# Kernel optimization log

Measured on AMD Instinct MI355X. Metric: run time of the kernel, lower is better.

Reference implementation:

```python
import jax, jax.numpy as jnp
import numpy as np

B, T, D, H, C = 2048, 512, 1, 50, 2  # batch, seq_len, input_size, hidden_size, num_classes


def setup_inputs() -> dict:
    key = jax.random.key(0)
    ks = jax.random.split(key, 11)
    k = 1.0 / np.sqrt(H)  # torch default init bound
    u = lambda kk, shape: jax.random.uniform(kk, shape, jnp.float32, -k, k)
    return {
        "x": jax.random.normal(ks[0], (B, T, D), jnp.float32),
        "W_ih0": u(ks[1], (4 * H, D)),
        "W_hh0": u(ks[2], (4 * H, H)),
        "b_ih0": u(ks[3], (4 * H,)),
        "b_hh0": u(ks[4], (4 * H,)),
        "W_ih1": u(ks[5], (4 * H, H)),
        "W_hh1": u(ks[6], (4 * H, H)),
        "b_ih1": u(ks[7], (4 * H,)),
        "b_hh1": u(ks[8], (4 * H,)),
        "W_fc": u(ks[9], (C, H)),
        "b_fc": u(ks[10], (C,)),
    }


def _lstm_layer(x, Wih, Whh, bih, bhh):
    # x: [B, T, Din] -> hidden sequence [B, T, H]. PyTorch gate order: i, f, g, o.
    Bn = x.shape[0]
    Hn = Whh.shape[1]
    # precompute input contribution for all timesteps (one big GEMM)
    xg = jnp.einsum('btd,gd->btg', x, Wih) + bih + bhh  # [B, T, 4H]

    def step(carry, xg_t):
        h, c = carry
        g = xg_t + h @ Whh.T  # [B, 4H]
        i, f, gg, o = jnp.split(g, 4, axis=-1)
        i = jax.nn.sigmoid(i)
        f = jax.nn.sigmoid(f)
        gg = jnp.tanh(gg)
        o = jax.nn.sigmoid(o)
        c = f * c + i * gg
        h = o * jnp.tanh(c)
        return (h, c), h

    h0 = jnp.zeros((Bn, Hn), x.dtype)
    c0 = jnp.zeros((Bn, Hn), x.dtype)
    (_, _), hs = jax.lax.scan(step, (h0, c0), jnp.swapaxes(xg, 0, 1))  # hs: [T, B, H]
    return jnp.swapaxes(hs, 0, 1)


def reference(x, W_ih0, W_hh0, b_ih0, b_hh0, W_ih1, W_hh1, b_ih1, b_hh1, W_fc, b_fc):
    h1 = _lstm_layer(x, W_ih0, W_hh0, b_ih0, b_hh0)
    h2 = _lstm_layer(h1, W_ih1, W_hh1, b_ih1, b_hh1)
    # out[:, -1, :] @ W_fc.T + b_fc  (last-timestep hidden -> classifier)
    return h2[:, -1, :] @ W_fc.T + b_fc
```

## Files before the change

### kernel.cpp

```cpp
#include <hip/hip_runtime.h>

#define T_SEQ 512
#define HID   50
#define NB    8
#define BLK   832

typedef float v4f  __attribute__((ext_vector_type(4)));
typedef _Float16 f16;
typedef f16  f16x8 __attribute__((ext_vector_type(8)));


__device__ __forceinline__ f16x8 ldA0(const float* __restrict__ Whh0,
                                      const float* __restrict__ Wih0,
                                      const float* __restrict__ bih0,
                                      const float* __restrict__ bhh0,
                                      int m, int kb) {
    const int u = m >> 2, g = m & 3;
    f16x8 v;
    #pragma unroll
    for (int j = 0; j < 8; ++j) {
        const int k = kb + j;
        float f = 0.f;
        if (u < HID) {
            const int rho = g * HID + u;
            if (k < HID)      f = Whh0[rho * HID + k];
            else if (k == 62) f = Wih0[rho];
            else if (k == 63) f = bih0[rho] + bhh0[rho];
        }
        v[j] = (f16)f;
    }
    return v;
}

__device__ __forceinline__ f16x8 ldA1a(const float* __restrict__ Wih1,
                                       const float* __restrict__ bih1,
                                       const float* __restrict__ bhh1,
                                       int m, int kb) {
    const int u = m >> 2, g = m & 3;
    f16x8 v;
    #pragma unroll
    for (int j = 0; j < 8; ++j) {
        const int k = kb + j;
        float f = 0.f;
        if (u < HID) {
            const int rho = g * HID + u;
            if (k < HID)      f = Wih1[rho * HID + k];
            else if (k == 63) f = bih1[rho] + bhh1[rho];
        }
        v[j] = (f16)f;
    }
    return v;
}

__device__ __forceinline__ f16x8 ldA1b(const float* __restrict__ Whh1,
                                       int m, int kb) {
    const int u = m >> 2, g = m & 3;
    f16x8 v;
    #pragma unroll
    for (int j = 0; j < 8; ++j) {
        const int k = kb + j;
        float f = 0.f;
        if (u < HID && k < HID) f = Whh1[(g * HID + u) * HID + k];
        v[j] = (f16)f;
    }
    return v;
}

#define MFMA16(A, B, C) __builtin_amdgcn_mfma_f32_16x16x32_f16((A), (B), (C), 0, 0, 0)

__global__ __launch_bounds__(BLK, 1)
void lstm2_mfma(const float* __restrict__ x,
                const float* __restrict__ Wih0,
                const float* __restrict__ Whh0,
                const float* __restrict__ bih0,
                const float* __restrict__ bhh0,
                const float* __restrict__ Wih1,
                const float* __restrict__ Whh1,
                const float* __restrict__ bih1,
                const float* __restrict__ bhh1,
                const float* __restrict__ Wfc,
                const float* __restrict__ bfc,
                float* __restrict__ out)
{
    __shared__ __align__(16) f16 BPH [8 * 64 * 8];
    __shared__ f16   xs16[NB][T_SEQ];
    __shared__ float hfin[HID][NB];

    const int tid  = threadIdx.x;
    const int w    = tid >> 6;
    const int lane = tid & 63;
    const int n16  = lane & 15;
    const int quad = lane >> 4;
    const int bb0  = blockIdx.x * NB;

    const float* xg = x + (long)bb0 * T_SEQ;

    for (int i = tid; i < 8 * 64 * 8; i += BLK) BPH[i] = (f16)0.f;
    for (int i = tid; i < NB * T_SEQ; i += BLK) {
        const int n = i >> 9, tt = i & (T_SEQ - 1);
        xs16[n][tt] = (f16)xg[n * T_SEQ + tt];
    }

    const int m   = w * 16 + n16;
    const int kb0 = quad * 8, kb1 = 32 + quad * 8;
    const f16x8 a0 = ldA0(Whh0, Wih0, bih0, bhh0, m, kb0);
    const f16x8 a1 = ldA0(Whh0, Wih0, bih0, bhh0, m, kb1);
    const f16x8 v0 = ldA1a(Wih1, bih1, bhh1, m, kb0);
    const f16x8 v1 = ldA1a(Wih1, bih1, bhh1, m, kb1);
    const f16x8 v2 = ldA1b(Whh1, m, kb0);
    const f16x8 v3 = ldA1b(Whh1, m, kb1);

    __syncthreads();
    if (tid < NB) {
        BPH[(1 * 64 + 48 + tid) * 8 + 7] = (f16)1.f;
        BPH[(1 * 64 + 56 + tid) * 8 + 7] = (f16)1.f;
        BPH[(3 * 64 + 48 + tid) * 8 + 7] = (f16)1.f;
        BPH[(3 * 64 + 56 + tid) * 8 + 7] = (f16)1.f;
        BPH[(3 * 64 + 48 + tid) * 8 + 6] = xs16[tid][0];
        BPH[(3 * 64 + 56 + tid) * 8 + 6] = xs16[tid][0];
    }
    __syncthreads();

    const int  u_    = w * 4 + quad;
    const bool isl0  = (n16 < 8);
    const bool valid = (u_ < HID);
    const int  wbase = (((u_ & 31) >> 3) * 16 + (n16 & 7)) * 8 + (u_ & 7) + (u_ >> 5) * 512;
    float cs = 0.f;
    const f16x8* BPF = (const f16x8*)BPH;
    const v4f CZ = {0.f, 0.f, 0.f, 0.f};

    #pragma clang loop unroll(disable)
    for (int s = 0; s <= T_SEQ; ++s) {
        const int rb = (s + 1) & 1, wb = s & 1;

        const f16x8 B0 = BPF[(2 * rb + 0) * 64 + lane];
        const f16x8 B1 = BPF[(2 * rb + 1) * 64 + lane];
        const f16x8 B2 = BPF[(4 + 2 * wb + 0) * 64 + lane];
        const f16x8 B3 = BPF[(4 + 2 * wb + 1) * 64 + lane];

        v4f C0 = MFMA16(a0, B0, CZ);
        C0 = MFMA16(a1, B1, C0);
        v4f C1h = MFMA16(v0, B0, CZ);
        C1h = MFMA16(v1, B1, C1h);
        v4f C1r = MFMA16(v2, B2, CZ);
        C1r = MFMA16(v3, B3, C1r);

        v4f CC;
        CC.x = isl0 ? C0.x : (C1h.x + C1r.x);
        CC.y = isl0 ? C0.y : (C1h.y + C1r.y);
        CC.z = isl0 ? C0.z : (C1h.z + C1r.z);
        CC.w = isl0 ? C0.w : (C1h.w + C1r.w);

        const bool active = isl0 ? (s < T_SEQ) : (s >= 1);

        const float e1 = __expf(-CC.x);
        const float e2 = __expf(-CC.y);
        const float e3 = __expf(-2.f * CC.z);
        const float e4 = __expf(-CC.w);
        const float d1 = 1.f + e1, d2 = 1.f + e2, d3 = 1.f + e3, d4 = 1.f + e4;
        const float p2 = d1 * d2, p3 = p2 * d3, p4 = p3 * d4;
        const float i4 = __builtin_amdgcn_rcpf(p4);
        const float go = i4 * p3;
        const float i3 = i4 * d4;
        const float r3 = i3 * p2;
        const float i2 = i3 * d3;
        const float gf = i2 * d1;
        const float gi = i2 * d2;
        const float gg = fmaf(2.f, r3, -1.f);
        const float csn = fmaf(gf, cs, gi * gg);
        cs = active ? csn : cs;
        const float th = fmaf(2.f, __builtin_amdgcn_rcpf(1.f + __expf(-2.f * cs)), -1.f);
        const float hh = go * th;

        if (valid && active) {
            const int tb = isl0 ? (2 * wb) : (4 + 2 * rb);
            f16* p = &BPH[tb * 512 + wbase];
            p[0]  = (f16)hh;
            p[64] = (f16)hh;
            if (!isl0 && s == T_SEQ) hfin[u_][n16 & 7] = hh;
        }

        if (w == 0 && lane < NB && s + 1 < T_SEQ) {
            const f16 xv = xs16[lane][s + 1];
            BPH[((2 * wb + 1) * 64 + 48 + lane) * 8 + 6] = xv;
            BPH[((2 * wb + 1) * 64 + 56 + lane) * 8 + 6] = xv;
        }

        __syncthreads();
    }

    if (tid < NB * 2) {
        const int nn = tid >> 1, c = tid & 1;
        float acc = bfc[c];
        #pragma unroll
        for (int u = 0; u < HID; ++u)
            acc = fmaf(Wfc[c * HID + u], hfin[u][nn], acc);
        out[(bb0 + nn) * 2 + c] = acc;
    }
}

extern "C" void kernel_launch(void* const* d_in, const int* in_sizes, int n_in,
                              void* d_out, int out_size, void* d_ws, size_t ws_size,
                              hipStream_t stream) {
    const float* x    = (const float*)d_in[0];
    const float* Wih0 = (const float*)d_in[1];
    const float* Whh0 = (const float*)d_in[2];
    const float* bih0 = (const float*)d_in[3];
    const float* bhh0 = (const float*)d_in[4];
    const float* Wih1 = (const float*)d_in[5];
    const float* Whh1 = (const float*)d_in[6];
    const float* bih1 = (const float*)d_in[7];
    const float* bhh1 = (const float*)d_in[8];
    const float* Wfc  = (const float*)d_in[9];
    const float* bfc  = (const float*)d_in[10];
    float* out = (float*)d_out;

    const int B = in_sizes[0] / T_SEQ;
    const int grid = B / NB;

    hipLaunchKernelGGL(lstm2_mfma, dim3(grid), dim3(BLK), 0, stream,
                       x, Wih0, Whh0, bih0, bhh0, Wih1, Whh1, bih1, bhh1,
                       Wfc, bfc, out);
}
```

Baseline: 369.8 us.

## Give each wave two M-tiles to halve wave count per block

The block shrinks from 13 to 7 waves, and each wave now handles two 16-row gate tiles instead of one. Each wave runs both tiles' MFMA chains and both gate nonlinearity pipelines, and it chains the layer-1 input and recurrent MFMAs into a single accumulator. The aim is to cut the per-step __syncthreads cost across fewer waves and to give each wave more independent work to interleave within the serial recurrence. In exchange, each wave carries twice the register pressure and a longer per-step instruction stream.

```diff
diff --git a/kernel.cpp b/kernel.cpp
--- a/kernel.cpp
+++ b/kernel.cpp
@@ -3,7 +3,7 @@
 #define T_SEQ 512
 #define HID   50
 #define NB    8
-#define BLK   832
+#define BLK   448
 
 typedef float v4f  __attribute__((ext_vector_type(4)));
 typedef _Float16 f16;
@@ -101,14 +101,21 @@
         xs16[n][tt] = (f16)xg[n * T_SEQ + tt];
     }
 
-    const int m   = w * 16 + n16;
+    const int m0  = (2 * w)     * 16 + n16;
+    const int m1  = (2 * w + 1) * 16 + n16;
     const int kb0 = quad * 8, kb1 = 32 + quad * 8;
-    const f16x8 a0 = ldA0(Whh0, Wih0, bih0, bhh0, m, kb0);
-    const f16x8 a1 = ldA0(Whh0, Wih0, bih0, bhh0, m, kb1);
-    const f16x8 v0 = ldA1a(Wih1, bih1, bhh1, m, kb0);
-    const f16x8 v1 = ldA1a(Wih1, bih1, bhh1, m, kb1);
-    const f16x8 v2 = ldA1b(Whh1, m, kb0);
-    const f16x8 v3 = ldA1b(Whh1, m, kb1);
+    const f16x8 a0  = ldA0(Whh0, Wih0, bih0, bhh0, m0, kb0);
+    const f16x8 a1  = ldA0(Whh0, Wih0, bih0, bhh0, m0, kb1);
+    const f16x8 a0p = ldA0(Whh0, Wih0, bih0, bhh0, m1, kb0);
+    const f16x8 a1p = ldA0(Whh0, Wih0, bih0, bhh0, m1, kb1);
+    const f16x8 v0  = ldA1a(Wih1, bih1, bhh1, m0, kb0);
+    const f16x8 v1  = ldA1a(Wih1, bih1, bhh1, m0, kb1);
+    const f16x8 v2  = ldA1b(Whh1, m0, kb0);
+    const f16x8 v3  = ldA1b(Whh1, m0, kb1);
+    const f16x8 v0p = ldA1a(Wih1, bih1, bhh1, m1, kb0);
+    const f16x8 v1p = ldA1a(Wih1, bih1, bhh1, m1, kb1);
+    const f16x8 v2p = ldA1b(Whh1, m1, kb0);
+    const f16x8 v3p = ldA1b(Whh1, m1, kb1);
 
     __syncthreads();
     if (tid < NB) {
@@ -121,11 +128,14 @@
     }
     __syncthreads();
 
-    const int  u_    = w * 4 + quad;
-    const bool isl0  = (n16 < 8);
-    const bool valid = (u_ < HID);
-    const int  wbase = (((u_ & 31) >> 3) * 16 + (n16 & 7)) * 8 + (u_ & 7) + (u_ >> 5) * 512;
-    float cs = 0.f;
+    const int  u_0    = 8 * w + quad;
+    const int  u_1    = 8 * w + 4 + quad;
+    const bool isl0   = (n16 < 8);
+    const bool valid0 = (u_0 < HID);
+    const bool valid1 = (u_1 < HID);
+    const int  wb0i   = (((u_0 & 31) >> 3) * 16 + (n16 & 7)) * 8 + (u_0 & 7) + (u_0 >> 5) * 512;
+    const int  wb1i   = (((u_1 & 31) >> 3) * 16 + (n16 & 7)) * 8 + (u_1 & 7) + (u_1 >> 5) * 512;
+    float cs0 = 0.f, cs1 = 0.f;
     const f16x8* BPF = (const f16x8*)BPH;
     const v4f CZ = {0.f, 0.f, 0.f, 0.f};
 
@@ -138,46 +148,61 @@
         const f16x8 B2 = BPF[(4 + 2 * wb + 0) * 64 + lane];
         const f16x8 B3 = BPF[(4 + 2 * wb + 1) * 64 + lane];
 
-        v4f C0 = MFMA16(a0, B0, CZ);
-        C0 = MFMA16(a1, B1, C0);
-        v4f C1h = MFMA16(v0, B0, CZ);
-        C1h = MFMA16(v1, B1, C1h);
-        v4f C1r = MFMA16(v2, B2, CZ);
-        C1r = MFMA16(v3, B3, C1r);
-
-        v4f CC;
-        CC.x = isl0 ? C0.x : (C1h.x + C1r.x);
-        CC.y = isl0 ? C0.y : (C1h.y + C1r.y);
-        CC.z = isl0 ? C0.z : (C1h.z + C1r.z);
-        CC.w = isl0 ? C0.w : (C1h.w + C1r.w);
+        v4f D0 = MFMA16(a0,  B0, CZ);  D0 = MFMA16(a1,  B1, D0);
+        v4f D1 = MFMA16(a0p, B0, CZ);  D1 = MFMA16(a1p, B1, D1);
+        v4f E0 = MFMA16(v0,  B0, CZ);  E0 = MFMA16(v1,  B1, E0);
+        E0 = MFMA16(v2,  B2, E0);      E0 = MFMA16(v3,  B3, E0);
+        v4f E1 = MFMA16(v0p, B0, CZ);  E1 = MFMA16(v1p, B1, E1);
+        E1 = MFMA16(v2p, B2, E1);      E1 = MFMA16(v3p, B3, E1);
+
+        v4f CA, CB;
+        CA.x = isl0 ? D0.x : E0.x;  CA.y = isl0 ? D0.y : E0.y;
+        CA.z = isl0 ? D0.z : E0.z;  CA.w = isl0 ? D0.w : E0.w;
+        CB.x = isl0 ? D1.x : E1.x;  CB.y = isl0 ? D1.y : E1.y;
+        CB.z = isl0 ? D1.z : E1.z;  CB.w = isl0 ? D1.w : E1.w;
 
         const bool active = isl0 ? (s < T_SEQ) : (s >= 1);
 
-        const float e1 = __expf(-CC.x);
-        const float e2 = __expf(-CC.y);
-        const float e3 = __expf(-2.f * CC.z);
-        const float e4 = __expf(-CC.w);
-        const float d1 = 1.f + e1, d2 = 1.f + e2, d3 = 1.f + e3, d4 = 1.f + e4;
-        const float p2 = d1 * d2, p3 = p2 * d3, p4 = p3 * d4;
-        const float i4 = __builtin_amdgcn_rcpf(p4);
-        const float go = i4 * p3;
-        const float i3 = i4 * d4;
-        const float r3 = i3 * p2;
-        const float i2 = i3 * d3;
-        const float gf = i2 * d1;
-        const float gi = i2 * d2;
-        const float gg = fmaf(2.f, r3, -1.f);
-        const float csn = fmaf(gf, cs, gi * gg);
-        cs = active ? csn : cs;
-        const float th = fmaf(2.f, __builtin_amdgcn_rcpf(1.f + __expf(-2.f * cs)), -1.f);
-        const float hh = go * th;
-
-        if (valid && active) {
+        const float e1a = __expf(-CA.x),        e1b = __expf(-CB.x);
+        const float e2a = __expf(-CA.y),        e2b = __expf(-CB.y);
+        const float e3a = __expf(-2.f * CA.z),  e3b = __expf(-2.f * CB.z);
+        const float e4a = __expf(-CA.w),        e4b = __expf(-CB.w);
+        const float d1a = 1.f + e1a, d2a = 1.f + e2a, d3a = 1.f + e3a, d4a = 1.f + e4a;
+        const float d1b = 1.f + e1b, d2b = 1.f + e2b, d3b = 1.f + e3b, d4b = 1.f + e4b;
+        const float p2a = d1a * d2a, p3a = p2a * d3a, p4a = p3a * d4a;
+        const float p2b = d1b * d2b, p3b = p2b * d3b, p4b = p3b * d4b;
+        const float i4a = __builtin_amdgcn_rcpf(p4a);
+        const float i4b = __builtin_amdgcn_rcpf(p4b);
+        const float goa = i4a * p3a,            gob = i4b * p3b;
+        const float i3a = i4a * d4a,            i3b = i4b * d4b;
+        const float r3a = i3a * p2a,            r3b = i3b * p2b;
+        const float i2a = i3a * d3a,            i2b = i3b * d3b;
+        const float gfa = i2a * d1a,            gfb = i2b * d1b;
+        const float gia = i2a * d2a,            gib = i2b * d2b;
+        const float gga = fmaf(2.f, r3a, -1.f), ggb = fmaf(2.f, r3b, -1.f);
+        const float ca  = fmaf(gfa, cs0, gia * gga);
+        const float cbv = fmaf(gfb, cs1, gib * ggb);
+        cs0 = active ? ca  : cs0;
+        cs1 = active ? cbv : cs1;
+        const float tha = fmaf(2.f, __builtin_amdgcn_rcpf(1.f + __expf(-2.f * cs0)), -1.f);
+        const float thb = fmaf(2.f, __builtin_amdgcn_rcpf(1.f + __expf(-2.f * cs1)), -1.f);
+        const float hha = goa * tha;
+        const float hhb = gob * thb;
+
+        if (active) {
             const int tb = isl0 ? (2 * wb) : (4 + 2 * rb);
-            f16* p = &BPH[tb * 512 + wbase];
-            p[0]  = (f16)hh;
-            p[64] = (f16)hh;
-            if (!isl0 && s == T_SEQ) hfin[u_][n16 & 7] = hh;
+            if (valid0) {
+                f16* p = &BPH[tb * 512 + wb0i];
+                p[0]  = (f16)hha;
+                p[64] = (f16)hha;
+                if (!isl0 && s == T_SEQ) hfin[u_0][n16 & 7] = hha;
+            }
+            if (valid1) {
+                f16* p = &BPH[tb * 512 + wb1i];
+                p[0]  = (f16)hhb;
+                p[64] = (f16)hhb;
+                if (!isl0 && s == T_SEQ) hfin[u_1][n16 & 7] = hhb;
+            }
         }
 
         if (w == 0 && lane < NB && s + 1 < T_SEQ) {
```

New measurement: 398.6 us. 7.8% more time.
